# Optimization experiments

Hardware: AMD Instinct MI355X
Metric: run time of the kernel (lower is better)

## Reference

```python
import jax, jax.numpy as jnp
import numpy as np

T, N, F = 96, 1140, 64   # timesteps, nodes per graph, node feature dim
H = 32                    # GAT hidden channels
LH = 250                  # LSTM hidden
OUT = 2280                # per-head output
E = 22800                 # edges per graph


def setup_inputs() -> dict:
    key = jax.random.key(0)
    ks = jax.random.split(key, 32)
    s = lambda k, shape, fan: jax.random.normal(k, shape, jnp.float32) / np.sqrt(fan)
    inp = {}
    inp["nodes"] = jax.random.normal(ks[0], (T, N, F), jnp.float32)
    inp["edges_index"] = jax.random.randint(ks[1], (T, 2, E), 0, N)
    inp["edges_attr"] = jax.random.normal(ks[2], (T, E), jnp.float32)  # unused by forward (faithful)
    # GAT layer 1 (F -> H) and layer 2 (H -> H), heads=1
    inp["gat_W1"] = s(ks[3], (F, H), F)
    inp["gat_as1"] = s(ks[4], (H,), H)
    inp["gat_ad1"] = s(ks[5], (H,), H)
    inp["gat_b1"] = jnp.zeros((H,), jnp.float32)
    inp["gat_W2"] = s(ks[6], (H, H), H)
    inp["gat_as2"] = s(ks[7], (H,), H)
    inp["gat_ad2"] = s(ks[8], (H,), H)
    inp["gat_b2"] = jnp.zeros((H,), jnp.float32)
    # 2-layer LSTM, batch_first, batch=1, input = N*H
    IN0 = N * H
    inp["Wih0"] = s(ks[9], (4 * LH, IN0), IN0)
    inp["Whh0"] = s(ks[10], (4 * LH, LH), LH)
    inp["bih0"] = jnp.zeros((4 * LH,), jnp.float32)
    inp["bhh0"] = jnp.zeros((4 * LH,), jnp.float32)
    inp["Wih1"] = s(ks[11], (4 * LH, LH), LH)
    inp["Whh1"] = s(ks[12], (4 * LH, LH), LH)
    inp["bih1"] = jnp.zeros((4 * LH,), jnp.float32)
    inp["bhh1"] = jnp.zeros((4 * LH,), jnp.float32)
    # random initial states (original uses torch.randn in forward)
    inp["h0"] = jax.random.normal(ks[13], (2, 1, LH), jnp.float32)
    inp["c0"] = jax.random.normal(ks[14], (2, 1, LH), jnp.float32)
    for i in range(4):
        inp[f"fc{i+1}_W"] = s(ks[15 + 2 * i], (OUT, LH), LH)
        inp[f"fc{i+1}_b"] = jnp.zeros((OUT,), jnp.float32)
    return inp


def _gat_conv(x, src, dst, W, a_s, a_d, b, n):
    # GATConv, heads=1: h = xW; e_ij = LeakyReLU(a_s.h_src + a_d.h_dst);
    # softmax over edges sharing a destination; scatter-add aggregation.
    h = x @ W                                                   # [N, H]
    e = jax.nn.leaky_relu((h @ a_s)[src] + (h @ a_d)[dst], negative_slope=0.2)
    m = jax.ops.segment_max(e, dst, num_segments=n)
    ex = jnp.exp(e - m[dst])
    denom = jax.ops.segment_sum(ex, dst, num_segments=n)
    alpha = ex / denom[dst]
    return jax.ops.segment_sum(alpha[:, None] * h[src], dst, num_segments=n) + b


def _lstm_layer(xs, Wih, Whh, bih, bhh, h0, c0):
    # xs: [T, B, in]; torch gate order i, f, g, o
    def step(carry, x):
        h, c = carry
        g = x @ Wih.T + h @ Whh.T + bih + bhh
        i, f, gg, o = jnp.split(g, 4, axis=-1)
        c = jax.nn.sigmoid(f) * c + jax.nn.sigmoid(i) * jnp.tanh(gg)
        h = jax.nn.sigmoid(o) * jnp.tanh(c)
        return (h, c), h
    (_, _), ys = jax.lax.scan(step, (h0, c0), xs)
    return ys


def reference(nodes, edges_index, edges_attr, gat_W1, gat_as1, gat_ad1, gat_b1,
              gat_W2, gat_as2, gat_ad2, gat_b2,
              Wih0, Whh0, bih0, bhh0, Wih1, Whh1, bih1, bhh1, h0, c0,
              fc1_W, fc1_b, fc2_W, fc2_b, fc3_W, fc3_b, fc4_W, fc4_b):
    n = nodes.shape[1]
    loop = jnp.arange(n)  # self-loops (GATConv default add_self_loops=True)

    def per_graph(x, ei):
        src = jnp.concatenate([ei[0], loop])
        dst = jnp.concatenate([ei[1], loop])
        h = jax.nn.relu(_gat_conv(x, src, dst, gat_W1, gat_as1, gat_ad1, gat_b1, n))
        h = _gat_conv(h, src, dst, gat_W2, gat_as2, gat_ad2, gat_b2, n)
        return h.reshape(-1)

    seq = jax.vmap(per_graph)(nodes, edges_index)   # [T, N*H]
    xs = seq[:, None, :]                            # [T, 1, N*H] (batch=1)
    ys = _lstm_layer(xs, Wih0, Whh0, bih0, bhh0, h0[0], c0[0])
    ys = _lstm_layer(ys, Wih1, Whh1, bih1, bhh1, h0[1], c0[1])
    last = ys[-1]                                   # [1, LH]
    preds = [last @ fc1_W.T + fc1_b, last @ fc2_W.T + fc2_b,
             last @ fc3_W.T + fc3_b, last @ fc4_W.T + fc4_b]
    return jnp.stack(preds, axis=0).reshape(last.shape[0], 4, -1)  # [1, 4, 2280]
```

## Files before the change

kernel.cpp:

```cpp
#include <hip/hip_runtime.h>

#define T_ 96
#define N_ 1140
#define F_ 64
#define H_ 32
#define E_ 22800
#define LH_ 250
#define G4_ 1000
#define OUT_ 2280
#define KIN_ 36480
#define SPLITK 60
#define KC 32
#define BN 32

typedef _Float16 h2_t __attribute__((ext_vector_type(2)));

__device__ __forceinline__ float leaky02(float x){ return x > 0.f ? x : 0.2f*x; }
__device__ __forceinline__ float fsigm(float x){ return 1.f/(1.f + __expf(-x)); }
__device__ __forceinline__ float ftanh(float x){
  x = fminf(fmaxf(x, -15.f), 15.f);
  float t = __expf(2.f * x);
  return (t - 1.f) / (t + 1.f);
}
__device__ __forceinline__ unsigned packh2(float a, float b) {
  auto p = __builtin_amdgcn_cvt_pkrtz(a, b);
  return __builtin_bit_cast(unsigned, p);
}
__device__ __forceinline__ float fdot2u(unsigned w, unsigned h, float acc) {
  return __builtin_amdgcn_fdot2(__builtin_bit_cast(h2_t, w),
                                __builtin_bit_cast(h2_t, h), acc, false);
}

__device__ __forceinline__ void st_agent_u(unsigned* p, unsigned v) {
  __hip_atomic_store(p, v, __ATOMIC_RELAXED, __HIP_MEMORY_SCOPE_AGENT);
}
__device__ __forceinline__ unsigned ld_agent_u(const unsigned* p) {
  return __hip_atomic_load((unsigned*)p, __ATOMIC_RELAXED, __HIP_MEMORY_SCOPE_AGENT);
}
__device__ __forceinline__ void st_agent_i(int* p, int v) {
  __hip_atomic_store(p, v, __ATOMIC_RELAXED, __HIP_MEMORY_SCOPE_AGENT);
}
__device__ __forceinline__ int ld_agent_i(const int* p) {
  return __hip_atomic_load((int*)p, __ATOMIC_RELAXED, __HIP_MEMORY_SCOPE_AGENT);
}

__global__ void k_feat(const float* __restrict__ x, const float* __restrict__ W,
                       const float* __restrict__ as_, const float* __restrict__ ad_,
                       float* __restrict__ Hout, float* __restrict__ HS,
                       float* __restrict__ HD, int K) {
  __shared__ float Wl[64 * 32];
  __shared__ float asl[32], adl[32];
  int tid = threadIdx.x;
  for (int i = tid; i < K * H_; i += 256) Wl[i] = W[i];
  if (tid < 32) { asl[tid] = as_[tid]; adl[tid] = ad_[tid]; }
  __syncthreads();
  int row = blockIdx.x * 8 + (tid >> 5);
  int c = tid & 31;
  if (row >= T_ * N_) return;
  const float4* xr = (const float4*)(x + (size_t)row * K);
  float acc = 0.f;
  for (int k4 = 0; k4 < (K >> 2); ++k4) {
    float4 v = xr[k4];
    acc += v.x * Wl[(4 * k4 + 0) * H_ + c];
    acc += v.y * Wl[(4 * k4 + 1) * H_ + c];
    acc += v.z * Wl[(4 * k4 + 2) * H_ + c];
    acc += v.w * Wl[(4 * k4 + 3) * H_ + c];
  }
  Hout[(size_t)row * H_ + c] = acc;
  float ps = acc * asl[c], pd = acc * adl[c];
  #pragma unroll
  for (int off = 16; off > 0; off >>= 1) {
    ps += __shfl_xor(ps, off, 32);
    pd += __shfl_xor(pd, off, 32);
  }
  if (c == 0) { HS[row] = ps; HD[row] = pd; }
}

__global__ void k_count(const int* __restrict__ ei, int* __restrict__ counts) {
  int gid = blockIdx.x * blockDim.x + threadIdx.x;
  if (gid >= T_ * E_) return;
  int t = gid / E_; int k = gid - t * E_;
  int dst = ei[(size_t)t * 2 * E_ + E_ + k];
  atomicAdd(&counts[t * N_ + dst], 1);
}

__global__ void k_scan(const int* __restrict__ counts, int* __restrict__ offs,
                       int* __restrict__ cursor) {
  int t = blockIdx.x; int tid = threadIdx.x;
  int base = tid * 5;
  int v[5]; int s = 0;
  #pragma unroll
  for (int r = 0; r < 5; ++r) {
    int i = base + r;
    int c = (i < N_) ? counts[t * N_ + i] : 0;
    v[r] = c; s += c;
  }
  __shared__ int sh[256];
  sh[tid] = s; __syncthreads();
  for (int off = 1; off < 256; off <<= 1) {
    int add = (tid >= off) ? sh[tid - off] : 0;
    __syncthreads();
    sh[tid] += add;
    __syncthreads();
  }
  int run = sh[tid] - s;
  #pragma unroll
  for (int r = 0; r < 5; ++r) {
    int i = base + r;
    if (i < N_) { offs[t * (N_ + 1) + i] = run; cursor[t * N_ + i] = run; }
    run += v[r];
  }
  if (tid == 255) offs[t * (N_ + 1) + N_] = sh[255];
}

__global__ void k_fill(const int* __restrict__ ei, int* __restrict__ cursor,
                       int* __restrict__ elist) {
  int gid = blockIdx.x * blockDim.x + threadIdx.x;
  if (gid >= T_ * E_) return;
  int t = gid / E_; int k = gid - t * E_;
  int src = ei[(size_t)t * 2 * E_ + k];
  int dst = ei[(size_t)t * 2 * E_ + E_ + k];
  int pos = atomicAdd(&cursor[t * N_ + dst], 1);
  elist[(size_t)t * E_ + pos] = src;
}

__global__ void k_aggr(const float* __restrict__ Hf, const float* __restrict__ HS,
                       const float* __restrict__ HD, const int* __restrict__ offs,
                       const int* __restrict__ elist, const float* __restrict__ b,
                       float* __restrict__ Xout, int relu) {
  int gid = blockIdx.x * blockDim.x + threadIdx.x;
  int row = gid >> 5; int c = gid & 31;
  if (row >= T_ * N_) return;
  int t = row / N_; int i = row - t * N_;
  float hd_i = HD[row];
  float m = leaky02(HS[row] + hd_i);
  float s = 1.f;
  float acc = Hf[(size_t)row * H_ + c];
  int e0 = offs[t * (N_ + 1) + i], e1 = offs[t * (N_ + 1) + i + 1];
  const int* el = elist + (size_t)t * E_;
  const float* Ht = Hf + (size_t)t * N_ * H_;
  const float* HSt = HS + t * N_;
  float hsA = 0.f, hvA = 0.f;
  if (e0 < e1) {
    int srcA = el[e0];
    hsA = HSt[srcA];
    hvA = Ht[(size_t)srcA * H_ + c];
  }
  for (int e = e0; e < e1; ++e) {
    float hs = hsA, hv = hvA;
    if (e + 1 < e1) {
      int srcA = el[e + 1];
      hsA = HSt[srcA];
      hvA = Ht[(size_t)srcA * H_ + c];
    }
    float eg = leaky02(hs + hd_i);
    float mn = fmaxf(m, eg);
    float scl = __expf(m - mn);
    float p = __expf(eg - mn);
    s = s * scl + p;
    acc = acc * scl + p * hv;
    m = mn;
  }
  float val = acc / s + b[c];
  if (relu) val = fmaxf(val, 0.f);
  Xout[(size_t)row * H_ + c] = val;
}

__global__ void k_gemm(const float* __restrict__ X, const float* __restrict__ Wih,
                       float* __restrict__ Gpart) {
  __shared__ unsigned Xs[T_][KC / 2 + 1];
  __shared__ unsigned Ws[BN][KC / 2 + 1];
  int j0 = blockIdx.x * BN;
  int sp = blockIdx.y;
  int tid = threadIdx.x;
  int jj = tid & 7;
  int tt = tid >> 3;
  float acc[6][4] = {};
  int kbeg = sp * (KIN_ / SPLITK);
  int kend = kbeg + (KIN_ / SPLITK);
  for (int k0 = kbeg; k0 < kend; k0 += KC) {
    for (int idx = tid; idx < T_ * (KC / 2); idx += 128) {
      int tr = idx >> 4; int kk = idx & 15;
      const float2 v = *(const float2*)(X + (size_t)tr * KIN_ + k0 + 2 * kk);
      Xs[tr][kk] = packh2(v.x, v.y);
    }
    for (int idx = tid; idx < BN * (KC / 2); idx += 128) {
      int jr = idx >> 4; int kk = idx & 15;
      int j = j0 + jr;
      unsigned v = 0;
      if (j < G4_) {
        const float2 w = *(const float2*)(Wih + (size_t)j * KIN_ + k0 + 2 * kk);
        v = packh2(w.x, w.y);
      }
      Ws[jr][kk] = v;
    }
    __syncthreads();
    for (int kk = 0; kk < KC / 2; ++kk) {
      unsigned xv[6], wv[4];
      #pragma unroll
      for (int r = 0; r < 6; ++r) xv[r] = Xs[tt * 6 + r][kk];
      #pragma unroll
      for (int q = 0; q < 4; ++q) wv[q] = Ws[jj * 4 + q][kk];
      #pragma unroll
      for (int r = 0; r < 6; ++r)
        #pragma unroll
        for (int q = 0; q < 4; ++q)
          acc[r][q] = fdot2u(wv[q], xv[r], acc[r][q]);
    }
    __syncthreads();
  }
  #pragma unroll
  for (int r = 0; r < 6; ++r) {
    int t = tt * 6 + r;
    #pragma unroll
    for (int q = 0; q < 4; ++q) {
      int j = j0 + jj * 4 + q;
      if (j < G4_) Gpart[((size_t)sp * T_ + t) * 1024 + j] = acc[r][q];
    }
  }
}

__global__ void k_gred(const float* __restrict__ Gpart, const float* __restrict__ bih,
                       const float* __restrict__ bhh, float* __restrict__ G0) {
  int idx = blockIdx.x * blockDim.x + threadIdx.x;
  if (idx >= T_ * G4_) return;
  int t = idx / G4_; int jg = idx - t * G4_;
  int j = jg >> 2, g = jg & 3;
  int c = g * LH_ + j;
  float s = bih[c] + bhh[c];
  for (int sp = 0; sp < SPLITK; ++sp) s += Gpart[((size_t)sp * T_ + t) * 1024 + c];
  G0[idx] = s;
}

__global__ void __launch_bounds__(512, 2) k_lstm(
    const float* __restrict__ G0, const float* __restrict__ Whh0,
    const float* __restrict__ Wih1, const float* __restrict__ Whh1,
    const float* __restrict__ bih1, const float* __restrict__ bhh1,
    const float* __restrict__ h0in, const float* __restrict__ c0in,
    unsigned* __restrict__ hp,
    int* __restrict__ flags,
    float* __restrict__ ylast) {
  int tid = threadIdx.x;
  int bid = blockIdx.x;
  int wv = bid * 8 + (tid >> 6);
  int lane = tid & 63;
  int qg = lane >> 4;
  int ql = lane & 15;

  unsigned w0[4][8], wx1[4][8], wh1[4][8];
  float bs1[4], c0l[4], c1l[4];
  bool act[4];
  #pragma unroll
  for (int u = 0; u < 4; ++u) {
    int U = wv * 4 + u;
    act[u] = (U < LH_);
    int Uc = act[u] ? U : 0;
    size_t rb = (size_t)(qg * LH_ + Uc) * LH_;
    #pragma unroll
    for (int m = 0; m < 8; ++m) {
      int pi = m * 16 + ql;
      if (act[u] && pi < 125) {
        w0[u][m]  = packh2(Whh0[rb + 2 * pi], Whh0[rb + 2 * pi + 1]);
        wx1[u][m] = packh2(Wih1[rb + 2 * pi], Wih1[rb + 2 * pi + 1]);
        wh1[u][m] = packh2(Whh1[rb + 2 * pi], Whh1[rb + 2 * pi + 1]);
      } else { w0[u][m] = 0; wx1[u][m] = 0; wh1[u][m] = 0; }
    }
    bs1[u] = act[u] ? (bih1[qg * LH_ + Uc] + bhh1[qg * LH_ + Uc]) : 0.f;
    c0l[u] = act[u] ? c0in[Uc] : 0.f;
    c1l[u] = act[u] ? c0in[LH_ + Uc] : 0.f;
  }

  float gpre[4];
  #pragma unroll
  for (int u = 0; u < 4; ++u)
    gpre[u] = act[u] ? G0[0 * G4_ + (wv * 4 + u) * 4 + qg] : 0.f;

  for (int p = 0; p <= T_; ++p) {
    int rs = (p - 1) & 1, wslot = p & 1;
    unsigned x0p[8], h1p[8];
    if (p == 0) {
      #pragma unroll
      for (int m = 0; m < 8; ++m) {
        int pi = m * 16 + ql;
        x0p[m] = (pi < 125) ? packh2(h0in[2 * pi], h0in[2 * pi + 1]) : 0u;
      }
    } else {
      #pragma unroll
      for (int m = 0; m < 8; ++m)
        x0p[m] = ld_agent_u(&hp[rs * 256 + m * 16 + ql]);
      if (p == 1) {
        #pragma unroll
        for (int m = 0; m < 8; ++m) {
          int pi = m * 16 + ql;
          h1p[m] = (pi < 125) ? packh2(h0in[LH_ + 2 * pi], h0in[LH_ + 2 * pi + 1]) : 0u;
        }
      } else {
        #pragma unroll
        for (int m = 0; m < 8; ++m)
          h1p[m] = ld_agent_u(&hp[rs * 256 + 128 + m * 16 + ql]);
      }
    }

    if (p < T_) {
      float h0new[4];
      #pragma unroll
      for (int u = 0; u < 4; ++u) {
        float s = 0.f;
        #pragma unroll
        for (int m = 0; m < 8; ++m) s = fdot2u(w0[u][m], x0p[m], s);
        s += __shfl_xor(s, 1); s += __shfl_xor(s, 2);
        s += __shfl_xor(s, 4); s += __shfl_xor(s, 8);
        float pre = s + gpre[u];
        float a = (qg == 2) ? ftanh(pre) : fsigm(pre);
        float ai = __shfl(a, ql);
        float af = __shfl(a, 16 + ql);
        float ag = __shfl(a, 32 + ql);
        float ao = __shfl(a, 48 + ql);
        c0l[u] = af * c0l[u] + ai * ag;
        h0new[u] = act[u] ? (ao * ftanh(c0l[u])) : 0.f;
      }
      if (lane == 0) {
        st_agent_u(&hp[wslot * 256 + 2 * wv],     packh2(h0new[0], h0new[1]));
        st_agent_u(&hp[wslot * 256 + 2 * wv + 1], packh2(h0new[2], h0new[3]));
      }
    }
    if (p >= 1) {
      float h1new[4];
      #pragma unroll
      for (int u = 0; u < 4; ++u) {
        float s = 0.f;
        #pragma unroll
        for (int m = 0; m < 8; ++m) s = fdot2u(wx1[u][m], x0p[m], s);
        #pragma unroll
        for (int m = 0; m < 8; ++m) s = fdot2u(wh1[u][m], h1p[m], s);
        s += __shfl_xor(s, 1); s += __shfl_xor(s, 2);
        s += __shfl_xor(s, 4); s += __shfl_xor(s, 8);
        float pre = s + bs1[u];
        float a = (qg == 2) ? ftanh(pre) : fsigm(pre);
        float bi = __shfl(a, ql);
        float bf = __shfl(a, 16 + ql);
        float bg = __shfl(a, 32 + ql);
        float bo = __shfl(a, 48 + ql);
        c1l[u] = bf * c1l[u] + bi * bg;
        h1new[u] = act[u] ? (bo * ftanh(c1l[u])) : 0.f;
      }
      if (p - 1 == T_ - 1 && lane == 0) {
        #pragma unroll
        for (int u = 0; u < 4; ++u)
          if (act[u]) ylast[wv * 4 + u] = h1new[u];
      }
      if (lane == 0) {
        st_agent_u(&hp[wslot * 256 + 128 + 2 * wv],     packh2(h1new[0], h1new[1]));
        st_agent_u(&hp[wslot * 256 + 128 + 2 * wv + 1], packh2(h1new[2], h1new[3]));
      }
    }
    float gnext[4];
    #pragma unroll
    for (int u = 0; u < 4; ++u)
      gnext[u] = (p + 1 < T_ && act[u]) ? G0[(p + 1) * G4_ + (wv * 4 + u) * 4 + qg] : 0.f;
    if (p < T_) {
      __syncthreads();
      if (tid == 0) {
        asm volatile("s_waitcnt vmcnt(0)" ::: "memory");
        st_agent_i(&flags[bid], p + 1);
      }
      if (tid < 64) {
        int guard = 0;
        for (;;) {
          int f = ld_agent_i(&flags[lane & 7]);
          if (__ballot(f >= p + 1) == ~0ULL) break;
          if (++guard > (1 << 22)) break;
          __builtin_amdgcn_s_sleep(1);
        }
      }
      __syncthreads();
    }
    #pragma unroll
    for (int u = 0; u < 4; ++u) gpre[u] = gnext[u];
  }
}

__global__ void k_fc(const float* __restrict__ ylast,
                     const float* __restrict__ Wa, const float* __restrict__ ba,
                     const float* __restrict__ Wb, const float* __restrict__ bb,
                     const float* __restrict__ Wc, const float* __restrict__ bc,
                     const float* __restrict__ Wd, const float* __restrict__ bd,
                     float* __restrict__ out) {
  int wg = blockIdx.x * 4 + (threadIdx.x >> 6);
  int lane = threadIdx.x & 63;
  if (wg >= 4 * OUT_) return;
  int head = wg / OUT_, o = wg - head * OUT_;
  const float* W = head == 0 ? Wa : head == 1 ? Wb : head == 2 ? Wc : Wd;
  const float* b = head == 0 ? ba : head == 1 ? bb : head == 2 ? bc : bd;
  float s = 0.f;
  #pragma unroll
  for (int r = 0; r < 4; ++r) {
    int idx = r * 64 + lane;
    if (idx < LH_) s += ylast[idx] * W[(size_t)o * LH_ + idx];
  }
  #pragma unroll
  for (int off = 32; off > 0; off >>= 1) s += __shfl_xor(s, off, 64);
  if (lane == 0) out[wg] = s + b[o];
}

extern "C" void kernel_launch(void* const* d_in, const int* in_sizes, int n_in,
                              void* d_out, int out_size, void* d_ws, size_t ws_size,
                              hipStream_t stream) {
  const float* nodes = (const float*)d_in[0];
  const int*   ei    = (const int*)d_in[1];
  const float* W1    = (const float*)d_in[3];
  const float* as1   = (const float*)d_in[4];
  const float* ad1   = (const float*)d_in[5];
  const float* b1    = (const float*)d_in[6];
  const float* W2    = (const float*)d_in[7];
  const float* as2   = (const float*)d_in[8];
  const float* ad2   = (const float*)d_in[9];
  const float* b2    = (const float*)d_in[10];
  const float* Wih0  = (const float*)d_in[11];
  const float* Whh0  = (const float*)d_in[12];
  const float* bih0  = (const float*)d_in[13];
  const float* bhh0  = (const float*)d_in[14];
  const float* Wih1  = (const float*)d_in[15];
  const float* Whh1  = (const float*)d_in[16];
  const float* bih1  = (const float*)d_in[17];
  const float* bhh1  = (const float*)d_in[18];
  const float* h0    = (const float*)d_in[19];
  const float* c0    = (const float*)d_in[20];
  const float* fW1   = (const float*)d_in[21];
  const float* fb1   = (const float*)d_in[22];
  const float* fW2   = (const float*)d_in[23];
  const float* fb2   = (const float*)d_in[24];
  const float* fW3   = (const float*)d_in[25];
  const float* fb3   = (const float*)d_in[26];
  const float* fW4   = (const float*)d_in[27];
  const float* fb4   = (const float*)d_in[28];
  float* out = (float*)d_out;

  const size_t o_Gpart  = 0;
  const size_t o_H      = 0;
  const size_t o_HS     = 14008320;
  const size_t o_HD     = 14446080;
  const size_t o_X1     = 14883840;
  const size_t o_X2     = 28892160;
  const size_t o_counts = 42900480;
  const size_t o_offs   = 43338240;
  const size_t o_cursor = 43776512;
  const size_t o_elist  = 44214272;
  const size_t o_G0     = 52969472;
  const size_t o_hp     = 53353472;
  const size_t o_flags  = 53355520;
  const size_t o_ylast  = 53355776;
  const size_t total    = 53356800;
  if (ws_size < total) return;

  char* ws = (char*)d_ws;
  float*    Gpart  = (float*)(ws + o_Gpart);
  float*    Hbuf   = (float*)(ws + o_H);
  float*    HS     = (float*)(ws + o_HS);
  float*    HD     = (float*)(ws + o_HD);
  float*    X1     = (float*)(ws + o_X1);
  float*    X2     = (float*)(ws + o_X2);
  int*      counts = (int*)(ws + o_counts);
  int*      offs   = (int*)(ws + o_offs);
  int*      cursor = (int*)(ws + o_cursor);
  int*      elist  = (int*)(ws + o_elist);
  float*    G0     = (float*)(ws + o_G0);
  unsigned* hp     = (unsigned*)(ws + o_hp);
  int*      flags  = (int*)(ws + o_flags);
  float*    ylast  = (float*)(ws + o_ylast);

  (void)hipMemsetAsync(counts, 0, (size_t)T_ * N_ * 4, stream);
  (void)hipMemsetAsync(hp, 0, 2048, stream);
  (void)hipMemsetAsync(flags, 0, 256, stream);

  const int rows_grid8 = (T_ * N_ + 7) / 8;
  const int rows_grid = (T_ * N_ * H_) / 256;
  const int eg = (T_ * E_ + 255) / 256;

  k_feat<<<rows_grid8, 256, 0, stream>>>(nodes, W1, as1, ad1, Hbuf, HS, HD, F_);
  k_count<<<eg, 256, 0, stream>>>(ei, counts);
  k_scan<<<T_, 256, 0, stream>>>(counts, offs, cursor);
  k_fill<<<eg, 256, 0, stream>>>(ei, cursor, elist);
  k_aggr<<<rows_grid, 256, 0, stream>>>(Hbuf, HS, HD, offs, elist, b1, X1, 1);
  k_feat<<<rows_grid8, 256, 0, stream>>>(X1, W2, as2, ad2, Hbuf, HS, HD, H_);
  k_aggr<<<rows_grid, 256, 0, stream>>>(Hbuf, HS, HD, offs, elist, b2, X2, 0);
  k_gemm<<<dim3(32, SPLITK), 128, 0, stream>>>(X2, Wih0, Gpart);
  k_gred<<<(T_ * G4_ + 255) / 256, 256, 0, stream>>>(Gpart, bih0, bhh0, G0);
  k_lstm<<<8, 512, 0, stream>>>(G0, Whh0, Wih1, Whh1, bih1, bhh1, h0, c0,
                                hp, flags, ylast);
  k_fc<<<OUT_, 256, 0, stream>>>(ylast, fW1, fb1, fW2, fb2, fW3, fb3, fW4, fb4, out);
}
```

Baseline: 1.115 ms.

## Fuse GAT layer-2 feature transform into layer-1 aggregation, merge count into feat

The layer-1 aggregation kernel now applies the ReLU, the 32x32 layer-2 weight transform (via wave shuffles) and the attention-score projections in place. This removes a separate feature kernel and the round trip of the X1 intermediate through memory. The edge-count kernel is merged into the layer-1 feature kernel as extra blocks in one launch, and the three memsets collapse into one by making flags and counts adjacent. Kernel launches and global traffic go down, at the cost of more register and LDS use in the aggregation kernel.

New measurement: 1.086 ms. 2.6% less time.

```diff
diff --git a/kernel.cpp b/kernel.cpp
--- a/kernel.cpp
+++ b/kernel.cpp
@@ -12,6 +12,8 @@
 #define SPLITK 60
 #define KC 32
 #define BN 32
+#define FEATB 13680
+#define CNTB 8550
 
 typedef _Float16 h2_t __attribute__((ext_vector_type(2)));
 
@@ -44,22 +46,30 @@
   return __hip_atomic_load((int*)p, __ATOMIC_RELAXED, __HIP_MEMORY_SCOPE_AGENT);
 }
 
-__global__ void k_feat(const float* __restrict__ x, const float* __restrict__ W,
-                       const float* __restrict__ as_, const float* __restrict__ ad_,
-                       float* __restrict__ Hout, float* __restrict__ HS,
-                       float* __restrict__ HD, int K) {
-  __shared__ float Wl[64 * 32];
+__global__ void k_featcnt(const float* __restrict__ x, const float* __restrict__ W,
+                          const float* __restrict__ as_, const float* __restrict__ ad_,
+                          float* __restrict__ Hout, float* __restrict__ HS,
+                          float* __restrict__ HD,
+                          const int* __restrict__ ei, int* __restrict__ counts) {
+  int tid = threadIdx.x;
+  if (blockIdx.x >= FEATB) {
+    int gid = (blockIdx.x - FEATB) * 256 + tid;
+    if (gid >= T_ * E_) return;
+    int t = gid / E_; int k = gid - t * E_;
+    int dst = ei[(size_t)t * 2 * E_ + E_ + k];
+    atomicAdd(&counts[t * N_ + dst], 1);
+    return;
+  }
+  __shared__ float Wl[F_ * H_];
   __shared__ float asl[32], adl[32];
-  int tid = threadIdx.x;
-  for (int i = tid; i < K * H_; i += 256) Wl[i] = W[i];
+  for (int i = tid; i < F_ * H_; i += 256) Wl[i] = W[i];
   if (tid < 32) { asl[tid] = as_[tid]; adl[tid] = ad_[tid]; }
   __syncthreads();
   int row = blockIdx.x * 8 + (tid >> 5);
   int c = tid & 31;
-  if (row >= T_ * N_) return;
-  const float4* xr = (const float4*)(x + (size_t)row * K);
+  const float4* xr = (const float4*)(x + (size_t)row * F_);
   float acc = 0.f;
-  for (int k4 = 0; k4 < (K >> 2); ++k4) {
+  for (int k4 = 0; k4 < (F_ >> 2); ++k4) {
     float4 v = xr[k4];
     acc += v.x * Wl[(4 * k4 + 0) * H_ + c];
     acc += v.y * Wl[(4 * k4 + 1) * H_ + c];
@@ -74,14 +84,6 @@
     pd += __shfl_xor(pd, off, 32);
   }
   if (c == 0) { HS[row] = ps; HD[row] = pd; }
-}
-
-__global__ void k_count(const int* __restrict__ ei, int* __restrict__ counts) {
-  int gid = blockIdx.x * blockDim.x + threadIdx.x;
-  if (gid >= T_ * E_) return;
-  int t = gid / E_; int k = gid - t * E_;
-  int dst = ei[(size_t)t * 2 * E_ + E_ + k];
-  atomicAdd(&counts[t * N_ + dst], 1);
 }
 
 __global__ void k_scan(const int* __restrict__ counts, int* __restrict__ offs,
@@ -124,10 +126,73 @@
   elist[(size_t)t * E_ + pos] = src;
 }
 
+__global__ void k_aggrfeat(const float* __restrict__ Hf, const float* __restrict__ HS,
+                           const float* __restrict__ HD, const int* __restrict__ offs,
+                           const int* __restrict__ elist, const float* __restrict__ b,
+                           const float* __restrict__ W2, const float* __restrict__ as2,
+                           const float* __restrict__ ad2,
+                           float* __restrict__ H2, float* __restrict__ HS2,
+                           float* __restrict__ HD2) {
+  __shared__ float W2l[H_ * H_];
+  __shared__ float as2l[32], ad2l[32];
+  int tid = threadIdx.x;
+  for (int i = tid; i < H_ * H_; i += 256) W2l[i] = W2[i];
+  if (tid < 32) { as2l[tid] = as2[tid]; ad2l[tid] = ad2[tid]; }
+  __syncthreads();
+  int gid = blockIdx.x * 256 + tid;
+  int row = gid >> 5; int c = gid & 31;
+  if (row >= T_ * N_) return;
+  int t = row / N_; int i = row - t * N_;
+  float hd_i = HD[row];
+  float m = leaky02(HS[row] + hd_i);
+  float s = 1.f;
+  float acc = Hf[(size_t)row * H_ + c];
+  int e0 = offs[t * (N_ + 1) + i], e1 = offs[t * (N_ + 1) + i + 1];
+  const int* el = elist + (size_t)t * E_;
+  const float* Ht = Hf + (size_t)t * N_ * H_;
+  const float* HSt = HS + t * N_;
+  float hsA = 0.f, hvA = 0.f;
+  if (e0 < e1) {
+    int srcA = el[e0];
+    hsA = HSt[srcA];
+    hvA = Ht[(size_t)srcA * H_ + c];
+  }
+  for (int e = e0; e < e1; ++e) {
+    float hs = hsA, hv = hvA;
+    if (e + 1 < e1) {
+      int srcA = el[e + 1];
+      hsA = HSt[srcA];
+      hvA = Ht[(size_t)srcA * H_ + c];
+    }
+    float eg = leaky02(hs + hd_i);
+    float mn = fmaxf(m, eg);
+    float scl = __expf(m - mn);
+    float p = __expf(eg - mn);
+    s = s * scl + p;
+    acc = acc * scl + p * hv;
+    m = mn;
+  }
+  float val = fmaxf(acc / s + b[c], 0.f);
+  float acc2 = 0.f;
+  #pragma unroll
+  for (int cc = 0; cc < 32; ++cc) {
+    float xc = __shfl(val, cc, 32);
+    acc2 += xc * W2l[cc * H_ + c];
+  }
+  H2[(size_t)row * H_ + c] = acc2;
+  float ps = acc2 * as2l[c], pd = acc2 * ad2l[c];
+  #pragma unroll
+  for (int off = 16; off > 0; off >>= 1) {
+    ps += __shfl_xor(ps, off, 32);
+    pd += __shfl_xor(pd, off, 32);
+  }
+  if (c == 0) { HS2[row] = ps; HD2[row] = pd; }
+}
+
 __global__ void k_aggr(const float* __restrict__ Hf, const float* __restrict__ HS,
                        const float* __restrict__ HD, const int* __restrict__ offs,
                        const int* __restrict__ elist, const float* __restrict__ b,
-                       float* __restrict__ Xout, int relu) {
+                       float* __restrict__ Xout) {
   int gid = blockIdx.x * blockDim.x + threadIdx.x;
   int row = gid >> 5; int c = gid & 31;
   if (row >= T_ * N_) return;
@@ -161,9 +226,7 @@
     acc = acc * scl + p * hv;
     m = mn;
   }
-  float val = acc / s + b[c];
-  if (relu) val = fmaxf(val, 0.f);
-  Xout[(size_t)row * H_ + c] = val;
+  Xout[(size_t)row * H_ + c] = acc / s + b[c];
 }
 
 __global__ void k_gemm(const float* __restrict__ X, const float* __restrict__ Wih,
@@ -440,17 +503,19 @@
   const size_t o_H      = 0;
   const size_t o_HS     = 14008320;
   const size_t o_HD     = 14446080;
-  const size_t o_X1     = 14883840;
+  const size_t o_H2     = 14883840;
   const size_t o_X2     = 28892160;
-  const size_t o_counts = 42900480;
-  const size_t o_offs   = 43338240;
-  const size_t o_cursor = 43776512;
-  const size_t o_elist  = 44214272;
-  const size_t o_G0     = 52969472;
-  const size_t o_hp     = 53353472;
-  const size_t o_flags  = 53355520;
-  const size_t o_ylast  = 53355776;
-  const size_t total    = 53356800;
+  const size_t o_flags  = 42900480;
+  const size_t o_counts = 42900736;
+  const size_t o_offs   = 43338496;
+  const size_t o_cursor = 43776640;
+  const size_t o_elist  = 44214400;
+  const size_t o_G0     = 52969600;
+  const size_t o_hp     = 53353600;
+  const size_t o_ylast  = 53355648;
+  const size_t o_HS2    = 53356672;
+  const size_t o_HD2    = 53794432;
+  const size_t total    = 54232192;
   if (ws_size < total) return;
 
   char* ws = (char*)d_ws;
@@ -458,32 +523,30 @@
   float*    Hbuf   = (float*)(ws + o_H);
   float*    HS     = (float*)(ws + o_HS);
   float*    HD     = (float*)(ws + o_HD);
-  float*    X1     = (float*)(ws + o_X1);
+  float*    H2     = (float*)(ws + o_H2);
   float*    X2     = (float*)(ws + o_X2);
+  int*      flags  = (int*)(ws + o_flags);
   int*      counts = (int*)(ws + o_counts);
   int*      offs   = (int*)(ws + o_offs);
   int*      cursor = (int*)(ws + o_cursor);
   int*      elist  = (int*)(ws + o_elist);
   float*    G0     = (float*)(ws + o_G0);
   unsigned* hp     = (unsigned*)(ws + o_hp);
-  int*      flags  = (int*)(ws + o_flags);
   float*    ylast  = (float*)(ws + o_ylast);
-
-  (void)hipMemsetAsync(counts, 0, (size_t)T_ * N_ * 4, stream);
-  (void)hipMemsetAsync(hp, 0, 2048, stream);
-  (void)hipMemsetAsync(flags, 0, 256, stream);
-
-  const int rows_grid8 = (T_ * N_ + 7) / 8;
+  float*    HS2    = (float*)(ws + o_HS2);
+  float*    HD2    = (float*)(ws + o_HD2);
+
+  (void)hipMemsetAsync(ws + o_flags, 0, 256 + (size_t)T_ * N_ * 4, stream);
+
   const int rows_grid = (T_ * N_ * H_) / 256;
-  const int eg = (T_ * E_ + 255) / 256;
-
-  k_feat<<<rows_grid8, 256, 0, stream>>>(nodes, W1, as1, ad1, Hbuf, HS, HD, F_);
-  k_count<<<eg, 256, 0, stream>>>(ei, counts);
+
+  k_featcnt<<<FEATB + CNTB, 256, 0, stream>>>(nodes, W1, as1, ad1,
+                                              Hbuf, HS, HD, ei, counts);
   k_scan<<<T_, 256, 0, stream>>>(counts, offs, cursor);
-  k_fill<<<eg, 256, 0, stream>>>(ei, cursor, elist);
-  k_aggr<<<rows_grid, 256, 0, stream>>>(Hbuf, HS, HD, offs, elist, b1, X1, 1);
-  k_feat<<<rows_grid8, 256, 0, stream>>>(X1, W2, as2, ad2, Hbuf, HS, HD, H_);
-  k_aggr<<<rows_grid, 256, 0, stream>>>(Hbuf, HS, HD, offs, elist, b2, X2, 0);
+  k_fill<<<CNTB, 256, 0, stream>>>(ei, cursor, elist);
+  k_aggrfeat<<<rows_grid, 256, 0, stream>>>(Hbuf, HS, HD, offs, elist, b1,
+                                            W2, as2, ad2, H2, HS2, HD2);
+  k_aggr<<<rows_grid, 256, 0, stream>>>(H2, HS2, HD2, offs, elist, b2, X2);
   k_gemm<<<dim3(32, SPLITK), 128, 0, stream>>>(X2, Wih0, Gpart);
   k_gred<<<(T_ * G4_ + 255) / 256, 256, 0, stream>>>(Gpart, bih0, bhh0, G0);
   k_lstm<<<8, 512, 0, stream>>>(G0, Whh0, Wih1, Whh1, bih1, bhh1, h0, c0,
```
